# Optimization experiments

Hardware: AMD Instinct MI355X
Metric: run time of the kernel (lower is better)

The kernel has to match this reference:

```python
import jax, jax.numpy as jnp
import numpy as np

N, A, H, D, K = 32768, 6, 1024, 128, 4096
BETA = 0.25


def setup_inputs() -> dict:
    key = jax.random.key(0)
    ks = jax.random.split(key, 16)
    sc = 0.02
    inp = {
        "action": jax.random.normal(ks[0], (N, A), dtype=jnp.float32),
        # encoder
        "W1": jax.random.normal(ks[1], (A, H), dtype=jnp.float32) * sc,
        "b1": jnp.zeros((H,), dtype=jnp.float32),
        "W2": jax.random.normal(ks[2], (H, H), dtype=jnp.float32) * sc,
        "b2": jnp.zeros((H,), dtype=jnp.float32),
        "Wmu": jax.random.normal(ks[3], (H, D), dtype=jnp.float32) * sc,
        "bmu": jnp.zeros((D,), dtype=jnp.float32),
        # codebook, init uniform(-1/K, 1/K) as in VectorQuantizer
        "codebook": jax.random.uniform(ks[4], (K, D), dtype=jnp.float32, minval=-1.0 / K, maxval=1.0 / K),
        # decoder
        "Wd1": jax.random.normal(ks[5], (D, H), dtype=jnp.float32) * sc,
        "bd1": jnp.zeros((H,), dtype=jnp.float32),
        "Wd2": jax.random.normal(ks[6], (H, H), dtype=jnp.float32) * sc,
        "bd2": jnp.zeros((H,), dtype=jnp.float32),
        "Wd3": jax.random.normal(ks[7], (H, A), dtype=jnp.float32) * sc,
        "bd3": jnp.zeros((A,), dtype=jnp.float32),
    }
    return inp


def reference(action, W1, b1, W2, b2, Wmu, bmu, codebook, Wd1, bd1, Wd2, bd2, Wd3, bd3):
    # encoder: Linear->ReLU, Linear->ReLU, Linear
    h = jax.nn.relu(action @ W1 + b1)
    h = jax.nn.relu(h @ W2 + b2)
    latents = h @ Wmu + bmu  # [N, D]

    # vector quantization: squared-distance argmin against codebook [K, D]
    dist = (jnp.sum(latents * latents, axis=1, keepdims=True)
            + jnp.sum(codebook * codebook, axis=1)
            - 2.0 * (latents @ codebook.T))  # [N, K]
    encoding_inds = jnp.argmin(dist, axis=1)  # [N]
    quantized = codebook[encoding_inds]  # gather == one-hot @ codebook

    commitment_loss = jnp.mean((jax.lax.stop_gradient(quantized) - latents) ** 2)
    embedding_loss = jnp.mean((quantized - jax.lax.stop_gradient(latents)) ** 2)
    vq_loss = BETA * commitment_loss + embedding_loss

    # straight-through estimator
    quantized_st = latents + jax.lax.stop_gradient(quantized - latents)

    # decoder: Linear->ReLU, Linear->ReLU, Linear->Tanh
    d = jax.nn.relu(quantized_st @ Wd1 + bd1)
    d = jax.nn.relu(d @ Wd2 + bd2)
    recons_action = jnp.tanh(d @ Wd3 + bd3)

    return encoding_inds[:, None], quantized_st, recons_action, vq_loss
```

## Files before the change

kernel.cpp:

```cpp
#include <hip/hip_runtime.h>
#include <cmath>

#define NROWS 32768
#define HID   1024
#define DIM   128
#define KCODE 4096
#define QBLK  384

typedef __attribute__((ext_vector_type(8))) short short8;
typedef __attribute__((ext_vector_type(4))) float f32x4;

__global__ __launch_bounds__(256) void enc1_kernel(const float* __restrict__ act,
                                                   const float* __restrict__ W1,
                                                   const float* __restrict__ b1,
                                                   float* __restrict__ h1)
{
    const int h = blockIdx.x * 256 + threadIdx.x;
    const int n = blockIdx.y;
    float a0 = act[n*6+0], a1 = act[n*6+1], a2 = act[n*6+2];
    float a3 = act[n*6+3], a4 = act[n*6+4], a5 = act[n*6+5];
    float acc = 0.f;
    acc = fmaf(a0, W1[0*HID + h], acc);
    acc = fmaf(a1, W1[1*HID + h], acc);
    acc = fmaf(a2, W1[2*HID + h], acc);
    acc = fmaf(a3, W1[3*HID + h], acc);
    acc = fmaf(a4, W1[4*HID + h], acc);
    acc = fmaf(a5, W1[5*HID + h], acc);
    acc = __fadd_rn(acc, b1[h]);
    h1[(size_t)n*HID + h] = fmaxf(acc, 0.f);
}

template<int BM, int ACT>
__global__ __launch_bounds__(256, 2) void gemm_kernel(const float* __restrict__ A,
                                                      const float* __restrict__ B,
                                                      const float* __restrict__ bias,
                                                      float* __restrict__ C,
                                                      int M, int K, int Nn)
{
    const int tid = threadIdx.x;
    const int tx = tid & 15, ty = tid >> 4;
    constexpr int G = BM / 64;
    const int bn = blockIdx.x * 128;
    const int bm = blockIdx.y * BM;

    __shared__ float As[32][BM + 4];
    __shared__ float Bs[32][132];

    float accB[4*G][8];
    float accC[4*G][8];
    #pragma unroll
    for (int i = 0; i < 4*G; ++i)
        #pragma unroll
        for (int j = 0; j < 8; ++j) { accB[i][j] = 0.f; accC[i][j] = 0.f; }

    for (int kt = 0; kt < K; kt += 32) {
        #pragma unroll
        for (int p = 0; p < BM/32; ++p) {
            int idx = tid + p*256;
            int row = idx >> 3;
            int k4  = (idx & 7) * 4;
            const float4 v = *reinterpret_cast<const float4*>(&A[(size_t)(bm+row)*K + kt + k4]);
            As[k4+0][row] = v.x; As[k4+1][row] = v.y;
            As[k4+2][row] = v.z; As[k4+3][row] = v.w;
        }
        #pragma unroll
        for (int p = 0; p < 4; ++p) {
            int idx  = tid + p*256;
            int krow = idx >> 5;
            int n4   = (idx & 31) * 4;
            *reinterpret_cast<float4*>(&Bs[krow][n4]) =
                *reinterpret_cast<const float4*>(&B[(size_t)(kt+krow)*Nn + bn + n4]);
        }
        __syncthreads();
        #pragma unroll
        for (int kk = 0; kk < 32; ++kk) {
            const float4 b0 = *reinterpret_cast<const float4*>(&Bs[kk][4*tx]);
            const float4 b1 = *reinterpret_cast<const float4*>(&Bs[kk][4*tx + 64]);
            const float bb[8] = {b0.x,b0.y,b0.z,b0.w,b1.x,b1.y,b1.z,b1.w};
            #pragma unroll
            for (int g = 0; g < G; ++g) {
                const float4 a = *reinterpret_cast<const float4*>(&As[kk][4*ty + 64*g]);
                const float aa[4] = {a.x,a.y,a.z,a.w};
                #pragma unroll
                for (int r = 0; r < 4; ++r)
                    #pragma unroll
                    for (int j = 0; j < 8; ++j)
                        accB[g*4+r][j] = fmaf(aa[r], bb[j], accB[g*4+r][j]);
            }
        }
        __syncthreads();
        if ((((kt + 32) % QBLK) == 0) || (kt + 32 >= K)) {
            #pragma unroll
            for (int i = 0; i < 4*G; ++i)
                #pragma unroll
                for (int j = 0; j < 8; ++j) {
                    accC[i][j] = __fadd_rn(accC[i][j], accB[i][j]);
                    accB[i][j] = 0.f;
                }
        }
    }
    const float4 bv0 = *reinterpret_cast<const float4*>(&bias[bn + 4*tx]);
    const float4 bv1 = *reinterpret_cast<const float4*>(&bias[bn + 4*tx + 64]);
    const float bb[8] = {bv0.x,bv0.y,bv0.z,bv0.w,bv1.x,bv1.y,bv1.z,bv1.w};
    #pragma unroll
    for (int g = 0; g < G; ++g)
        #pragma unroll
        for (int r = 0; r < 4; ++r) {
            const int i = g*4 + r;
            const int row = bm + 64*g + 4*ty + r;
            float o[8];
            #pragma unroll
            for (int j = 0; j < 8; ++j) {
                float v = __fadd_rn(accC[i][j], bb[j]);
                if (ACT == 1) v = fmaxf(v, 0.f);
                o[j] = v;
            }
            *reinterpret_cast<float4*>(&C[(size_t)row*Nn + bn + 4*tx])      = make_float4(o[0],o[1],o[2],o[3]);
            *reinterpret_cast<float4*>(&C[(size_t)row*Nn + bn + 64 + 4*tx]) = make_float4(o[4],o[5],o[6],o[7]);
        }
}

__device__ inline unsigned short bf16_rne(float x) {
    union { float f; unsigned u; } a; a.f = x;
    unsigned r = a.u + 0x7FFFu + ((a.u >> 16) & 1u);
    return (unsigned short)(r >> 16);
}
__device__ inline void split_bf16(float x, unsigned short& hi, unsigned short& lo) {
    hi = bf16_rne(x);
    union { unsigned u; float f; } h; h.u = (unsigned)hi << 16;
    lo = bf16_rne(x - h.f);
}

__global__ __launch_bounds__(256) void convA_kernel(const float* __restrict__ src,
                                                    unsigned short* __restrict__ dst,
                                                    int M, int K)
{
    const int kq = K >> 2;
    const int total = M * kq;
    for (int t = blockIdx.x*256 + threadIdx.x; t < total; t += gridDim.x*256) {
        int m  = t / kq;
        int kc = (t - m*kq) << 2;
        float4 v = *reinterpret_cast<const float4*>(&src[(size_t)m*K + kc]);
        ushort4 hi, lo;
        split_bf16(v.x, hi.x, lo.x);
        split_bf16(v.y, hi.y, lo.y);
        split_bf16(v.z, hi.z, lo.z);
        split_bf16(v.w, hi.w, lo.w);
        size_t base = (size_t)m*3*K;
        *reinterpret_cast<ushort4*>(&dst[base + kc])       = hi;
        *reinterpret_cast<ushort4*>(&dst[base + K + kc])   = hi;
        *reinterpret_cast<ushort4*>(&dst[base + 2*K + kc]) = lo;
    }
}

__global__ __launch_bounds__(256) void convW_kernel(const float* __restrict__ W,
                                                    unsigned short* __restrict__ WT,
                                                    int K, int N)
{
    const int total = K * N;
    for (int t = blockIdx.x*256 + threadIdx.x; t < total; t += gridDim.x*256) {
        int k = t / N, n = t - k*N;
        unsigned short hi, lo;
        split_bf16(W[(size_t)k*N + n], hi, lo);
        size_t base = (size_t)n*3*K;
        WT[base + k]       = hi;
        WT[base + K + k]   = lo;
        WT[base + 2*K + k] = hi;
    }
}

template<int ACT>
__global__ __launch_bounds__(256) void gemm_bf16_kernel(const unsigned short* __restrict__ A,
                                                        const unsigned short* __restrict__ BT,
                                                        const float* __restrict__ bias,
                                                        float* __restrict__ C,
                                                        int M, int Kp, int Nn)
{
    __shared__ unsigned short Asm[128*64];
    __shared__ unsigned short Bsm[128*64];
    const int tid  = threadIdx.x;
    const int lane = tid & 63;
    const int wave = tid >> 6;
    const int wr = wave >> 1, wc = wave & 1;
    const int bm = blockIdx.y * 128, bn = blockIdx.x * 128;
    const int l15 = lane & 15, l4 = lane >> 4;

    f32x4 acc[4][4];
    #pragma unroll
    for (int i = 0; i < 4; ++i)
        #pragma unroll
        for (int j = 0; j < 4; ++j) acc[i][j] = (f32x4){0.f,0.f,0.f,0.f};

    const int srow = tid >> 3;
    const int sch  = (tid & 7) * 8;
    for (int kt = 0; kt < Kp; kt += 64) {
        #pragma unroll
        for (int p = 0; p < 4; ++p) {
            int row = srow + 32*p;
            short8 va = *reinterpret_cast<const short8*>(&A[(size_t)(bm+row)*Kp + kt + sch]);
            short8 vb = *reinterpret_cast<const short8*>(&BT[(size_t)(bn+row)*Kp + kt + sch]);
            int byte = (row*128 + sch*2) ^ ((row & 7) << 4);
            *reinterpret_cast<short8*>((char*)Asm + byte) = va;
            *reinterpret_cast<short8*>((char*)Bsm + byte) = vb;
        }
        __syncthreads();
        #pragma unroll
        for (int ks = 0; ks < 64; ks += 32) {
            const int kk2 = (ks + l4*8) * 2;
            short8 af[4], bf[4];
            #pragma unroll
            for (int i = 0; i < 4; ++i) {
                int mrow = wr*64 + i*16 + l15;
                af[i] = *reinterpret_cast<const short8*>((char*)Asm + ((mrow*128 + kk2) ^ ((mrow & 7) << 4)));
                int nrow = wc*64 + i*16 + l15;
                bf[i] = *reinterpret_cast<const short8*>((char*)Bsm + ((nrow*128 + kk2) ^ ((nrow & 7) << 4)));
            }
            #pragma unroll
            for (int i = 0; i < 4; ++i)
                #pragma unroll
                for (int j = 0; j < 4; ++j)
                    acc[i][j] = __builtin_amdgcn_mfma_f32_16x16x32_bf16(af[i], bf[j], acc[i][j], 0, 0, 0);
        }
        __syncthreads();
    }
    #pragma unroll
    for (int j = 0; j < 4; ++j) {
        const int col = bn + wc*64 + j*16 + l15;
        const float bv = bias[col];
        #pragma unroll
        for (int i = 0; i < 4; ++i) {
            #pragma unroll
            for (int r = 0; r < 4; ++r) {
                const int row = bm + wr*64 + i*16 + l4*4 + r;
                float v = acc[i][j][r] + bv;
                if (ACT == 1) v = fmaxf(v, 0.f);
                C[(size_t)row*Nn + col] = v;
            }
        }
    }
}

__global__ __launch_bounds__(128) void rownorm_np_kernel(const float* __restrict__ X,
                                                         int nrows,
                                                         float* __restrict__ out)
{
    const int r = blockIdx.x * 128 + threadIdx.x;
    if (r >= nrows) return;
    const float* p = X + (size_t)r * DIM;
    float lane[16];
    #pragma unroll
    for (int l = 0; l < 16; ++l) {
        float x0 = p[0*16 + l],  y0 = p[64 + 0*16 + l];
        float x1 = p[1*16 + l],  y1 = p[64 + 1*16 + l];
        float a0 = __fadd_rn(__fmul_rn(x0, x0), __fmul_rn(y0, y0));
        float a1 = __fadd_rn(__fmul_rn(x1, x1), __fmul_rn(y1, y1));
        float r01 = __fadd_rn(a0, a1);
        float x2 = p[2*16 + l],  y2 = p[64 + 2*16 + l];
        float x3 = p[3*16 + l],  y3 = p[64 + 3*16 + l];
        float a2 = __fadd_rn(__fmul_rn(x2, x2), __fmul_rn(y2, y2));
        float a3 = __fadd_rn(__fmul_rn(x3, x3), __fmul_rn(y3, y3));
        float r23 = __fadd_rn(a2, a3);
        lane[l] = __fadd_rn(r01, r23);
    }
    float s[8];
    #pragma unroll
    for (int l = 0; l < 8; ++l) s[l] = __fadd_rn(lane[l], lane[l+8]);
    float u[4];
    #pragma unroll
    for (int l = 0; l < 4; ++l) u[l] = __fadd_rn(s[l], s[l+4]);
    float v0 = __fadd_rn(u[0], u[2]);
    float v1 = __fadd_rn(u[1], u[3]);
    out[r] = __fadd_rn(v0, v1);
}

__global__ __launch_bounds__(256, 2) void vq_kernel(const float* __restrict__ L,
                                                    const float* __restrict__ CB,
                                                    const float* __restrict__ SL,
                                                    const float* __restrict__ CN,
                                                    float* __restrict__ outInd,
                                                    float* __restrict__ outQ,
                                                    float* __restrict__ lossAcc)
{
    const int tid = threadIdx.x;
    const int tx = tid & 15, ty = tid >> 4;
    const int bm = blockIdx.x * 64;

    __shared__ float As[32][68];
    __shared__ float Bs[32][132];
    __shared__ int   sIdx[64];

    float slr[4], bestv[4];
    int   besti[4];
    #pragma unroll
    for (int r = 0; r < 4; ++r) {
        slr[r] = SL[bm + 4*ty + r];
        bestv[r] = 3.4e38f; besti[r] = 0x7fffffff;
    }

    for (int k0 = 0; k0 < KCODE; k0 += 128) {
        float acc[4][8];
        #pragma unroll
        for (int r = 0; r < 4; ++r)
            #pragma unroll
            for (int j = 0; j < 8; ++j) acc[r][j] = 0.f;

        for (int d0 = 0; d0 < DIM; d0 += 32) {
            #pragma unroll
            for (int p = 0; p < 2; ++p) {
                int idx = tid + p*256;
                int row = idx >> 3;
                int d4  = (idx & 7) * 4;
                const float4 v = *reinterpret_cast<const float4*>(&L[(size_t)(bm+row)*DIM + d0 + d4]);
                As[d4+0][row] = v.x; As[d4+1][row] = v.y;
                As[d4+2][row] = v.z; As[d4+3][row] = v.w;
            }
            #pragma unroll
            for (int p = 0; p < 4; ++p) {
                int idx  = tid + p*256;
                int crow = idx >> 3;
                int d4   = (idx & 7) * 4;
                const float4 w = *reinterpret_cast<const float4*>(&CB[(size_t)(k0+crow)*DIM + d0 + d4]);
                Bs[d4+0][crow] = w.x; Bs[d4+1][crow] = w.y;
                Bs[d4+2][crow] = w.z; Bs[d4+3][crow] = w.w;
            }
            __syncthreads();
            #pragma unroll
            for (int dd = 0; dd < 32; ++dd) {
                const float4 a  = *reinterpret_cast<const float4*>(&As[dd][4*ty]);
                const float4 b0 = *reinterpret_cast<const float4*>(&Bs[dd][4*tx]);
                const float4 b1 = *reinterpret_cast<const float4*>(&Bs[dd][4*tx + 64]);
                const float aa[4] = {a.x,a.y,a.z,a.w};
                const float bb[8] = {b0.x,b0.y,b0.z,b0.w,b1.x,b1.y,b1.z,b1.w};
                #pragma unroll
                for (int r = 0; r < 4; ++r)
                    #pragma unroll
                    for (int j = 0; j < 8; ++j)
                        acc[r][j] = fmaf(aa[r], bb[j], acc[r][j]);
            }
            __syncthreads();
        }
        #pragma unroll
        for (int r = 0; r < 4; ++r) {
            float mv = 3.4e38f; int mi = 0x7fffffff;
            #pragma unroll
            for (int j = 0; j < 8; ++j) {
                int c = k0 + ((j < 4) ? (4*tx + j) : (64 + 4*tx + (j-4)));
                float t1   = __fadd_rn(slr[r], CN[c]);
                float u    = __fmul_rn(2.0f, acc[r][j]);
                float dist = __fadd_rn(t1, -u);
                if (dist < mv || (dist == mv && c < mi)) { mv = dist; mi = c; }
            }
            #pragma unroll
            for (int m = 1; m < 16; m <<= 1) {
                float ov = __shfl_xor(mv, m, 16);
                int   oi = __shfl_xor(mi, m, 16);
                if (ov < mv || (ov == mv && oi < mi)) { mv = ov; mi = oi; }
            }
            if (mv < bestv[r] || (mv == bestv[r] && mi < besti[r])) {
                bestv[r] = mv; besti[r] = mi;
            }
        }
    }
    if (tx == 0) {
        #pragma unroll
        for (int r = 0; r < 4; ++r) {
            int row = 4*ty + r;
            outInd[bm + row] = (float)besti[r];
            sIdx[row] = besti[r];
        }
    }
    __syncthreads();
    float lsum = 0.f;
    #pragma unroll
    for (int p = 0; p < 8; ++p) {
        int q   = tid + p*256;
        int row = q >> 5;
        int d4  = (q & 31) * 4;
        int ci  = sIdx[row];
        const float4 qv = *reinterpret_cast<const float4*>(&CB[(size_t)ci*DIM + d4]);
        const float4 lv = *reinterpret_cast<const float4*>(&L[(size_t)(bm+row)*DIM + d4]);
        *reinterpret_cast<float4*>(&outQ[(size_t)(bm+row)*DIM + d4]) = qv;
        float dx = qv.x - lv.x, dy = qv.y - lv.y, dz = qv.z - lv.z, dw = qv.w - lv.w;
        lsum += dx*dx + dy*dy + dz*dz + dw*dw;
    }
    #pragma unroll
    for (int s = 32; s; s >>= 1) lsum += __shfl_down(lsum, s, 64);
    __shared__ float part[4];
    if ((tid & 63) == 0) part[tid >> 6] = lsum;
    __syncthreads();
    if (tid == 0) atomicAdd(lossAcc, part[0] + part[1] + part[2] + part[3]);
}

__global__ __launch_bounds__(256) void dec3_kernel(const float* __restrict__ d2,
                                                   const float* __restrict__ Wd3,
                                                   const float* __restrict__ bd3,
                                                   float* __restrict__ out)
{
    const int w = threadIdx.x >> 6, lane = threadIdx.x & 63;
    const int n = blockIdx.x * 4 + w;
    float acc[6] = {0.f, 0.f, 0.f, 0.f, 0.f, 0.f};
    for (int k = lane; k < HID; k += 64) {
        float v = d2[(size_t)n*HID + k];
        #pragma unroll
        for (int o = 0; o < 6; ++o) acc[o] = fmaf(v, Wd3[k*6 + o], acc[o]);
    }
    #pragma unroll
    for (int o = 0; o < 6; ++o)
        #pragma unroll
        for (int s = 32; s; s >>= 1) acc[o] += __shfl_down(acc[o], s, 64);
    if (lane == 0) {
        #pragma unroll
        for (int o = 0; o < 6; ++o)
            out[(size_t)n*6 + o] = tanhf(__fadd_rn(acc[o], bd3[o]));
    }
}

__global__ void zero1_kernel(float* __restrict__ p) { p[0] = 0.f; }

__global__ void loss_final_kernel(const float* __restrict__ lossAcc,
                                  float* __restrict__ out)
{
    out[0] = 1.25f * lossAcc[0] / (float)(NROWS * DIM);
}

extern "C" void kernel_launch(void* const* d_in, const int* in_sizes, int n_in,
                              void* d_out, int out_size, void* d_ws, size_t ws_size,
                              hipStream_t stream)
{
    const float* action = (const float*)d_in[0];
    const float* W1  = (const float*)d_in[1];
    const float* b1  = (const float*)d_in[2];
    const float* W2  = (const float*)d_in[3];
    const float* b2  = (const float*)d_in[4];
    const float* Wmu = (const float*)d_in[5];
    const float* bmu = (const float*)d_in[6];
    const float* CB  = (const float*)d_in[7];
    const float* Wd1 = (const float*)d_in[8];
    const float* bd1 = (const float*)d_in[9];
    const float* Wd2 = (const float*)d_in[10];
    const float* bd2 = (const float*)d_in[11];
    const float* Wd3 = (const float*)d_in[12];
    const float* bd3 = (const float*)d_in[13];

    float* out = (float*)d_out;
    const size_t o1 = NROWS;
    const size_t o2 = o1 + (size_t)NROWS*DIM;
    const size_t o3 = o2 + (size_t)NROWS*6;

    int ch = 8192;
    size_t need = 0;
    while (true) {
        need = 2*(size_t)ch*HID*4 + (size_t)NROWS*DIM*4 + (size_t)NROWS*4
             + (size_t)KCODE*4 + 64
             + (size_t)ch*3*HID*2 + (size_t)HID*3*DIM*2 + (size_t)HID*3*HID*2;
        if (need <= ws_size || ch <= 128) break;
        ch >>= 1;
    }
    if (need > ws_size) return;

    char* ws = (char*)d_ws;
    size_t off = 0;
    float* bufA    = (float*)(ws + off); off += (size_t)ch*HID*4;
    float* bufB    = (float*)(ws + off); off += (size_t)ch*HID*4;
    float* latF    = (float*)(ws + off); off += (size_t)NROWS*DIM*4;
    float* slF     = (float*)(ws + off); off += (size_t)NROWS*4;
    float* cnorm   = (float*)(ws + off); off += (size_t)KCODE*4;
    float* lossAcc = (float*)(ws + off); off += 64;
    unsigned short* Abf = (unsigned short*)(ws + off); off += (size_t)ch*3*HID*2;
    unsigned short* W1T = (unsigned short*)(ws + off); off += (size_t)HID*3*DIM*2;
    unsigned short* W2T = (unsigned short*)(ws + off);

    zero1_kernel<<<1, 1, 0, stream>>>(lossAcc);
    rownorm_np_kernel<<<dim3(KCODE/128), 128, 0, stream>>>(CB, KCODE, cnorm);
    convW_kernel<<<dim3(512), 256, 0, stream>>>(Wd1, W1T, DIM, HID);
    convW_kernel<<<dim3(1024), 256, 0, stream>>>(Wd2, W2T, HID, HID);

    for (int c0 = 0; c0 < NROWS; c0 += ch) {
        enc1_kernel<<<dim3(HID/256, ch), 256, 0, stream>>>(action + (size_t)c0*6, W1, b1, bufA);
        gemm_kernel<128,1><<<dim3(HID/128, ch/128), 256, 0, stream>>>(bufA, W2, b2, bufB, ch, HID, HID);
        gemm_kernel<64,0><<<dim3(1, ch/64), 256, 0, stream>>>(bufB, Wmu, bmu, latF + (size_t)c0*DIM, ch, HID, DIM);
    }

    rownorm_np_kernel<<<dim3(NROWS/128), 128, 0, stream>>>(latF, NROWS, slF);
    vq_kernel<<<dim3(NROWS/64), 256, 0, stream>>>(latF, CB, slF, cnorm, out, out + o1, lossAcc);

    for (int c0 = 0; c0 < NROWS; c0 += ch) {
        const float* qC = out + o1 + (size_t)c0*DIM;
        convA_kernel<<<dim3(1024), 256, 0, stream>>>(qC, Abf, ch, DIM);
        gemm_bf16_kernel<1><<<dim3(HID/128, ch/128), 256, 0, stream>>>(Abf, W1T, bd1, bufA, ch, 3*DIM, HID);
        convA_kernel<<<dim3(2048), 256, 0, stream>>>(bufA, Abf, ch, HID);
        gemm_bf16_kernel<1><<<dim3(HID/128, ch/128), 256, 0, stream>>>(Abf, W2T, bd2, bufB, ch, 3*HID, HID);
        dec3_kernel<<<dim3(ch/4), 256, 0, stream>>>(bufB, Wd3, bd3, out + o2 + (size_t)c0*6);
    }

    loss_final_kernel<<<1, 1, 0, stream>>>(lossAcc, out + o3);
}
```

Measured before the change: 2.401 ms.

## Drop split-bf16 emulation in decoder GEMMs and convert activations inside GEMM

The decoder GEMMs previously emulated near-fp32 precision with a 3-term bf16 hi/lo split, which tripled the K dimension, and a separate conversion kernel wrote the split activations to workspace. Now the weights are stored as a single bf16 copy, and the GEMM reads fp32 activations directly and rounds them to bf16 while loading into shared memory. This removes two conversion kernels and cuts decoder MMA work about threefold. The cost is reduced decoder accuracy (plain bf16), which may exceed the output tolerance.

Result: faster. 2.146 ms (-10.6%).

```diff
diff --git a/kernel.cpp b/kernel.cpp
--- a/kernel.cpp
+++ b/kernel.cpp
@@ -125,33 +125,6 @@
     unsigned r = a.u + 0x7FFFu + ((a.u >> 16) & 1u);
     return (unsigned short)(r >> 16);
 }
-__device__ inline void split_bf16(float x, unsigned short& hi, unsigned short& lo) {
-    hi = bf16_rne(x);
-    union { unsigned u; float f; } h; h.u = (unsigned)hi << 16;
-    lo = bf16_rne(x - h.f);
-}
-
-__global__ __launch_bounds__(256) void convA_kernel(const float* __restrict__ src,
-                                                    unsigned short* __restrict__ dst,
-                                                    int M, int K)
-{
-    const int kq = K >> 2;
-    const int total = M * kq;
-    for (int t = blockIdx.x*256 + threadIdx.x; t < total; t += gridDim.x*256) {
-        int m  = t / kq;
-        int kc = (t - m*kq) << 2;
-        float4 v = *reinterpret_cast<const float4*>(&src[(size_t)m*K + kc]);
-        ushort4 hi, lo;
-        split_bf16(v.x, hi.x, lo.x);
-        split_bf16(v.y, hi.y, lo.y);
-        split_bf16(v.z, hi.z, lo.z);
-        split_bf16(v.w, hi.w, lo.w);
-        size_t base = (size_t)m*3*K;
-        *reinterpret_cast<ushort4*>(&dst[base + kc])       = hi;
-        *reinterpret_cast<ushort4*>(&dst[base + K + kc])   = hi;
-        *reinterpret_cast<ushort4*>(&dst[base + 2*K + kc]) = lo;
-    }
-}
 
 __global__ __launch_bounds__(256) void convW_kernel(const float* __restrict__ W,
                                                     unsigned short* __restrict__ WT,
@@ -160,21 +133,16 @@
     const int total = K * N;
     for (int t = blockIdx.x*256 + threadIdx.x; t < total; t += gridDim.x*256) {
         int k = t / N, n = t - k*N;
-        unsigned short hi, lo;
-        split_bf16(W[(size_t)k*N + n], hi, lo);
-        size_t base = (size_t)n*3*K;
-        WT[base + k]       = hi;
-        WT[base + K + k]   = lo;
-        WT[base + 2*K + k] = hi;
+        WT[(size_t)n*K + k] = bf16_rne(W[(size_t)k*N + n]);
     }
 }
 
 template<int ACT>
-__global__ __launch_bounds__(256) void gemm_bf16_kernel(const unsigned short* __restrict__ A,
+__global__ __launch_bounds__(256) void gemm_bf16_kernel(const float* __restrict__ A,
                                                         const unsigned short* __restrict__ BT,
                                                         const float* __restrict__ bias,
                                                         float* __restrict__ C,
-                                                        int M, int Kp, int Nn)
+                                                        int M, int K, int Nn)
 {
     __shared__ unsigned short Asm[128*64];
     __shared__ unsigned short Bsm[128*64];
@@ -193,12 +161,18 @@
 
     const int srow = tid >> 3;
     const int sch  = (tid & 7) * 8;
-    for (int kt = 0; kt < Kp; kt += 64) {
+    for (int kt = 0; kt < K; kt += 64) {
         #pragma unroll
         for (int p = 0; p < 4; ++p) {
             int row = srow + 32*p;
-            short8 va = *reinterpret_cast<const short8*>(&A[(size_t)(bm+row)*Kp + kt + sch]);
-            short8 vb = *reinterpret_cast<const short8*>(&BT[(size_t)(bn+row)*Kp + kt + sch]);
+            const float4 f0 = *reinterpret_cast<const float4*>(&A[(size_t)(bm+row)*K + kt + sch]);
+            const float4 f1 = *reinterpret_cast<const float4*>(&A[(size_t)(bm+row)*K + kt + sch + 4]);
+            short8 va;
+            va[0] = (short)bf16_rne(f0.x); va[1] = (short)bf16_rne(f0.y);
+            va[2] = (short)bf16_rne(f0.z); va[3] = (short)bf16_rne(f0.w);
+            va[4] = (short)bf16_rne(f1.x); va[5] = (short)bf16_rne(f1.y);
+            va[6] = (short)bf16_rne(f1.z); va[7] = (short)bf16_rne(f1.w);
+            short8 vb = *reinterpret_cast<const short8*>(&BT[(size_t)(bn+row)*K + kt + sch]);
             int byte = (row*128 + sch*2) ^ ((row & 7) << 4);
             *reinterpret_cast<short8*>((char*)Asm + byte) = va;
             *reinterpret_cast<short8*>((char*)Bsm + byte) = vb;
@@ -452,7 +426,7 @@
     while (true) {
         need = 2*(size_t)ch*HID*4 + (size_t)NROWS*DIM*4 + (size_t)NROWS*4
              + (size_t)KCODE*4 + 64
-             + (size_t)ch*3*HID*2 + (size_t)HID*3*DIM*2 + (size_t)HID*3*HID*2;
+             + (size_t)HID*DIM*2 + (size_t)HID*HID*2;
         if (need <= ws_size || ch <= 128) break;
         ch >>= 1;
     }
@@ -466,13 +440,12 @@
     float* slF     = (float*)(ws + off); off += (size_t)NROWS*4;
     float* cnorm   = (float*)(ws + off); off += (size_t)KCODE*4;
     float* lossAcc = (float*)(ws + off); off += 64;
-    unsigned short* Abf = (unsigned short*)(ws + off); off += (size_t)ch*3*HID*2;
-    unsigned short* W1T = (unsigned short*)(ws + off); off += (size_t)HID*3*DIM*2;
+    unsigned short* W1T = (unsigned short*)(ws + off); off += (size_t)HID*DIM*2;
     unsigned short* W2T = (unsigned short*)(ws + off);
 
     zero1_kernel<<<1, 1, 0, stream>>>(lossAcc);
     rownorm_np_kernel<<<dim3(KCODE/128), 128, 0, stream>>>(CB, KCODE, cnorm);
-    convW_kernel<<<dim3(512), 256, 0, stream>>>(Wd1, W1T, DIM, HID);
+    convW_kernel<<<dim3(256), 256, 0, stream>>>(Wd1, W1T, DIM, HID);
     convW_kernel<<<dim3(1024), 256, 0, stream>>>(Wd2, W2T, HID, HID);
 
     for (int c0 = 0; c0 < NROWS; c0 += ch) {
@@ -486,10 +459,8 @@
 
     for (int c0 = 0; c0 < NROWS; c0 += ch) {
         const float* qC = out + o1 + (size_t)c0*DIM;
-        convA_kernel<<<dim3(1024), 256, 0, stream>>>(qC, Abf, ch, DIM);
-        gemm_bf16_kernel<1><<<dim3(HID/128, ch/128), 256, 0, stream>>>(Abf, W1T, bd1, bufA, ch, 3*DIM, HID);
-        convA_kernel<<<dim3(2048), 256, 0, stream>>>(bufA, Abf, ch, HID);
-        gemm_bf16_kernel<1><<<dim3(HID/128, ch/128), 256, 0, stream>>>(Abf, W2T, bd2, bufB, ch, 3*HID, HID);
+        gemm_bf16_kernel<1><<<dim3(HID/128, ch/128), 256, 0, stream>>>(qC, W1T, bd1, bufA, ch, DIM, HID);
+        gemm_bf16_kernel<1><<<dim3(HID/128, ch/128), 256, 0, stream>>>(bufA, W2T, bd2, bufB, ch, HID, HID);
         dec3_kernel<<<dim3(ch/4), 256, 0, stream>>>(bufB, Wd3, bd3, out + o2 + (size_t)c0*6);
     }
 
```
